# Performance work log

Measured on AMD Instinct MI355X. Metric: run time of the kernel, lower is better.

The kernel has to match this reference:

```python
import jax, jax.numpy as jnp
import numpy as np

EMBED_DIM = 128
MAX_ATOM_TYPE = 119
N_ATOMS = 1048576


def setup_inputs() -> dict:
    key = jax.random.key(0)
    k1, k2, k3 = jax.random.split(key, 3)
    atom_type = jax.random.randint(k1, (N_ATOMS,), 0, MAX_ATOM_TYPE)
    # nn.Linear(max_atom_type, embed_dim): weight [embed_dim, max_atom_type], bias [embed_dim]
    bound = 1.0 / np.sqrt(MAX_ATOM_TYPE)
    W = jax.random.uniform(k2, (EMBED_DIM, MAX_ATOM_TYPE), minval=-bound, maxval=bound, dtype=jnp.float32)
    b = jax.random.uniform(k3, (EMBED_DIM,), minval=-bound, maxval=bound, dtype=jnp.float32)
    return {"atom_type": atom_type, "W": W, "b": b}


def reference(atom_type, W, b):
    # one_hot(atom_type) @ W.T + b  ==  gather rows of W.T (columns of W) + bias
    # [N, embed_dim]
    return jnp.take(W.T, atom_type, axis=0) + b
```

## Files before the change

### kernel.cpp

```cpp
#include <hip/hip_runtime.h>

#define EMBED_DIM 128
#define MAX_ATOM_TYPE 119
#define TABLE_ELEMS (MAX_ATOM_TYPE * EMBED_DIM)

__global__ __launch_bounds__(256) void embed_atom_kernel(
    const int* __restrict__ atom_type,
    const float* __restrict__ W,
    const float* __restrict__ bias,
    float* __restrict__ out,
    int n_atoms)
{
    __shared__ float table[TABLE_ELEMS];

    for (int i = threadIdx.x; i < TABLE_ELEMS; i += 256) {
        int t = i >> 7;
        int d = i & 127;
        table[i] = W[d * MAX_ATOM_TYPE + t] + bias[d];
    }
    __syncthreads();

    const float4* tab4 = reinterpret_cast<const float4*>(table);
    float4* out4 = reinterpret_cast<float4*>(out);

    const long long total_f4 = (long long)n_atoms * (EMBED_DIM / 4);
    const long long stride   = (long long)gridDim.x * blockDim.x;

    for (long long pos = (long long)blockIdx.x * blockDim.x + threadIdx.x;
         pos < total_f4; pos += stride) {
        int atom = (int)(pos >> 5);
        int d4   = (int)(pos & 31);
        int t    = atom_type[atom];
        out4[pos] = tab4[t * (EMBED_DIM / 4) + d4];
    }
}

extern "C" void kernel_launch(void* const* d_in, const int* in_sizes, int n_in,
                              void* d_out, int out_size, void* d_ws, size_t ws_size,
                              hipStream_t stream) {
    const int*   atom_type = (const int*)d_in[0];
    const float* W         = (const float*)d_in[1];
    const float* bias      = (const float*)d_in[2];
    float*       out       = (float*)d_out;
    int n_atoms = in_sizes[0];

    int blocks = 2048;
    embed_atom_kernel<<<blocks, 256, 0, stream>>>(atom_type, W, bias, out, n_atoms);
}
```

Measured before the change: 652.2 us.

## Prebuild transposed table in workspace, batch loads, use nontemporal stores

A small pre-kernel builds the transposed, bias-added table in workspace once, so each block of the main kernel only copies it into shared memory with contiguous vector loads. The main kernel uses 1024-thread blocks, a grid sized at 16 float4 per thread, and issues batches of 8 index loads before the table lookups. Output is written with nontemporal stores to avoid polluting cache. This adds a second kernel launch, and a padded fallback path runs when no workspace is available.

```diff
diff --git a/kernel.cpp b/kernel.cpp
--- a/kernel.cpp
+++ b/kernel.cpp
@@ -1,37 +1,93 @@
 #include <hip/hip_runtime.h>
 
-#define EMBED_DIM 128
-#define MAX_ATOM_TYPE 119
-#define TABLE_ELEMS (MAX_ATOM_TYPE * EMBED_DIM)
+#define ED 128
+#define NT 119
+#define TE (NT * ED)
+#define BLK 1024
+#define BATCH 8
 
-__global__ __launch_bounds__(256) void embed_atom_kernel(
+typedef float f32x4 __attribute__((ext_vector_type(4)));
+
+__global__ __launch_bounds__(256) void build_table(
+    const float* __restrict__ W,
+    const float* __restrict__ bias,
+    float* __restrict__ T)
+{
+    int i = blockIdx.x * 256 + threadIdx.x;
+    if (i < TE) {
+        int t = i >> 7;
+        int d = i & 127;
+        T[i] = W[d * NT + t] + bias[d];
+    }
+}
+
+__global__ __launch_bounds__(BLK) void embed_main(
+    const int* __restrict__ atom_type,
+    const float* __restrict__ T,
+    float* __restrict__ out,
+    long long total_f4)
+{
+    __shared__ f32x4 tab4[TE / 4];
+
+    const f32x4* Tg = reinterpret_cast<const f32x4*>(T);
+    for (int i = threadIdx.x; i < TE / 4; i += BLK) tab4[i] = Tg[i];
+    __syncthreads();
+
+    f32x4* out4 = reinterpret_cast<f32x4*>(out);
+    const long long stride = (long long)gridDim.x * BLK;
+    const long long base   = (long long)blockIdx.x * BLK + threadIdx.x;
+
+    long long pos = base;
+    for (; pos + (BATCH - 1) * stride < total_f4; pos += BATCH * stride) {
+        int   t[BATCH];
+        f32x4 v[BATCH];
+#pragma unroll
+        for (int k = 0; k < BATCH; ++k) {
+            long long p = pos + (long long)k * stride;
+            t[k] = atom_type[(int)(p >> 5)];
+        }
+#pragma unroll
+        for (int k = 0; k < BATCH; ++k) {
+            long long p = pos + (long long)k * stride;
+            v[k] = tab4[t[k] * 32 + (int)(p & 31)];
+        }
+#pragma unroll
+        for (int k = 0; k < BATCH; ++k) {
+            long long p = pos + (long long)k * stride;
+            __builtin_nontemporal_store(v[k], &out4[p]);
+        }
+    }
+    for (; pos < total_f4; pos += stride) {
+        int t = atom_type[(int)(pos >> 5)];
+        __builtin_nontemporal_store(tab4[t * 32 + (int)(pos & 31)], &out4[pos]);
+    }
+}
+
+#define PAD 132
+__global__ __launch_bounds__(BLK) void embed_fallback(
     const int* __restrict__ atom_type,
     const float* __restrict__ W,
     const float* __restrict__ bias,
     float* __restrict__ out,
-    int n_atoms)
+    long long total_f4)
 {
-    __shared__ float table[TABLE_ELEMS];
+    __shared__ __align__(16) float tab[NT * PAD];
 
-    for (int i = threadIdx.x; i < TABLE_ELEMS; i += 256) {
-        int t = i >> 7;
-        int d = i & 127;
-        table[i] = W[d * MAX_ATOM_TYPE + t] + bias[d];
+    for (int j = threadIdx.x; j < TE; j += BLK) {
+        int d = j / NT;
+        int t = j - d * NT;
+        tab[t * PAD + d] = W[j] + bias[d];
     }
     __syncthreads();
 
-    const float4* tab4 = reinterpret_cast<const float4*>(table);
-    float4* out4 = reinterpret_cast<float4*>(out);
-
-    const long long total_f4 = (long long)n_atoms * (EMBED_DIM / 4);
-    const long long stride   = (long long)gridDim.x * blockDim.x;
-
-    for (long long pos = (long long)blockIdx.x * blockDim.x + threadIdx.x;
+    f32x4* out4 = reinterpret_cast<f32x4*>(out);
+    const long long stride = (long long)gridDim.x * BLK;
+    for (long long pos = (long long)blockIdx.x * BLK + threadIdx.x;
          pos < total_f4; pos += stride) {
-        int atom = (int)(pos >> 5);
-        int d4   = (int)(pos & 31);
-        int t    = atom_type[atom];
-        out4[pos] = tab4[t * (EMBED_DIM / 4) + d4];
+        int t  = atom_type[(int)(pos >> 5)];
+        int d4 = (int)(pos & 31);
+        f32x4 v = *reinterpret_cast<const f32x4*>(&tab[t * PAD + d4 * 4]);
+        __builtin_nontemporal_store(v, &out4[pos]);
     }
 }
 
@@ -42,8 +98,20 @@
     const float* W         = (const float*)d_in[1];
     const float* bias      = (const float*)d_in[2];
     float*       out       = (float*)d_out;
-    int n_atoms = in_sizes[0];
+    int n_atoms = (n_in > 0) ? in_sizes[0] : 0;
+    if (n_atoms <= 0) return;
 
-    int blocks = 2048;
-    embed_atom_kernel<<<blocks, 256, 0, stream>>>(atom_type, W, bias, out, n_atoms);
+    long long total_f4 = (long long)n_atoms * (ED / 4);
+
+    if (ws_size >= (size_t)TE * sizeof(float)) {
+        float* T = (float*)d_ws;
+        build_table<<<(TE + 255) / 256, 256, 0, stream>>>(W, bias, T);
+        long long blocks = (total_f4 + (long long)BLK * 16 - 1) / ((long long)BLK * 16);
+        if (blocks < 1) blocks = 1;
+        embed_main<<<(int)blocks, BLK, 0, stream>>>(atom_type, T, out, total_f4);
+    } else {
+        long long blocks = (total_f4 + (long long)BLK * 16 - 1) / ((long long)BLK * 16);
+        if (blocks < 1) blocks = 1;
+        embed_fallback<<<(int)blocks, BLK, 0, stream>>>(atom_type, W, bias, out, total_f4);
+    }
 }
```

Measured after the change: 545.6 us. 1.2x faster.
